# Performance work log

Hardware: AMD Instinct MI355X
Metric: run time of the kernel (lower is better)

The kernel has to match this reference:

```python
import jax, jax.numpy as jnp
import numpy as np

N = 50000
NEG_SLOPE = 0.2

def _gat_layer(x, src, dst, W, a_src, a_dst, b):
    # x: [N, Fin], W: [Fin, Fout], a_src/a_dst: [Fout], b: [Fout]
    h = x @ W                                  # [N, Fout]
    alpha_src = h @ a_src                      # [N]
    alpha_dst = h @ a_dst                      # [N]
    e = alpha_src[src] + alpha_dst[dst]        # [E]
    e = jnp.where(e > 0, e, NEG_SLOPE * e)     # leaky_relu
    # segment softmax over incoming edges of each dst node
    m = jax.ops.segment_max(e, dst, num_segments=N)
    w = jnp.exp(e - m[dst])
    denom = jax.ops.segment_sum(w, dst, num_segments=N) + jnp.asarray(1e-16, e.dtype)
    alpha = w / denom[dst]                     # [E]
    out = jax.ops.segment_sum(alpha[:, None] * h[src], dst, num_segments=N)
    return out + b

def setup_inputs() -> dict:
    key = jax.random.key(0)
    ks = jax.random.split(key, 10)
    x = jax.random.normal(ks[0], (N, 128), dtype=jnp.float32)
    edge_index = jax.random.randint(ks[1], (2, 800000), 0, N, dtype=jnp.int64)
    def glorot(k, shape):
        fan = shape[0] + (shape[1] if len(shape) > 1 else 1)
        s = jnp.sqrt(6.0 / fan)
        return jax.random.uniform(k, shape, jnp.float32, -s, s)
    return {
        "x": x,
        "edge_index": edge_index,
        "W1": glorot(ks[2], (128, 64)),
        "a1_src": glorot(ks[3], (64,)),
        "a1_dst": glorot(ks[4], (64,)),
        "b1": jnp.zeros((64,), jnp.float32),
        "W2": glorot(ks[5], (64, 64)),
        "a2_src": glorot(ks[6], (64,)),
        "a2_dst": glorot(ks[7], (64,)),
        "b2": jnp.zeros((64,), jnp.float32),
    }

def reference(x, edge_index, W1, a1_src, a1_dst, b1, W2, a2_src, a2_dst, b2):
    loops = jnp.arange(N, dtype=edge_index.dtype)
    src = jnp.concatenate([edge_index[0], loops])  # add self-loops (PyG default)
    dst = jnp.concatenate([edge_index[1], loops])
    h = _gat_layer(x, src, dst, W1, a1_src, a1_dst, b1)
    h = jax.nn.relu(h)
    out = _gat_layer(h, src, dst, W2, a2_src, a2_dst, b2)
    return out
```

## Files before the change

### kernel.cpp

```cpp
#include <hip/hip_runtime.h>
#include <hip/hip_bf16.h>
#include <hip/hip_fp16.h>
#include <cstddef>


#define NNODES 50000
#define NEDGES 800000
#define FOUT   64
#define NBKT   512
#define BSPAN  98
#define CHUNK  4096
#define REGS   2560
#define NLBMAX 256

__device__ __forceinline__ float leaky(float t) { return t > 0.f ? t : 0.2f * t; }
#define RL(v, j) __builtin_amdgcn_readlane((v), (j))

using half8  = __attribute__((ext_vector_type(8))) _Float16;
using half4v = __attribute__((ext_vector_type(4))) _Float16;
using f32x4  = __attribute__((ext_vector_type(4))) float;


__global__ __launch_bounds__(256) void k_localsort(
    const int* __restrict__ ei, unsigned* __restrict__ gout,
    int* __restrict__ goff, int E)
{
    __shared__ unsigned lrec[CHUNK];
    __shared__ unsigned lsrt[CHUNK];
    __shared__ int cnt[NBKT];
    __shared__ int cur[NBKT];
    __shared__ int exc[NBKT + 1];

    const int t = threadIdx.x;
    const int blk = blockIdx.x;
    const int e0 = blk * CHUNK;
    const int e1 = min(e0 + CHUNK, E);
    const int ne = e1 - e0;

    for (int i = t; i < NBKT; i += 256) cnt[i] = 0;
    __syncthreads();

    for (int i = e0 + t; i < e1; i += 256) {
        unsigned s = (unsigned)ei[i];
        unsigned d = (unsigned)ei[E + i];
        lrec[i - e0] = s | (d << 16);
        atomicAdd(&cnt[d / BSPAN], 1);
    }
    __syncthreads();

    if (t < 64) {
        int c[8]; int s = 0;
        #pragma unroll
        for (int k = 0; k < 8; ++k) { c[k] = cnt[t * 8 + k]; s += c[k]; }
        int inc = s;
        #pragma unroll
        for (int d = 1; d < 64; d <<= 1) { int u = __shfl_up(inc, d); if (t >= d) inc += u; }
        int ex = inc - s;
        #pragma unroll
        for (int k = 0; k < 8; ++k) { exc[t * 8 + k] = ex; cur[t * 8 + k] = ex; ex += c[k]; }
        if (t == 63) exc[NBKT] = ex;
    }
    __syncthreads();

    for (int i = t; i < ne; i += 256) {
        unsigned r = lrec[i];
        unsigned d = r >> 16;
        unsigned b = d / BSPAN;
        int p = atomicAdd(&cur[b], 1);
        lsrt[p] = (r & 0xFFFFu) | ((d - b * BSPAN) << 16);
    }
    __syncthreads();

    for (int i = t; i < ne; i += 256) gout[e0 + i] = lsrt[i];
    for (int i = t; i < NBKT + 1; i += 256)
        goff[blk * (NBKT + 1) + i] = e0 + exc[i];
}


__device__ __forceinline__ void csr_body(
    char* smem, int bkt,
    const unsigned* __restrict__ gout, const int* __restrict__ goff,
    int* __restrict__ csrc, int2* __restrict__ rowse,
    int n, int nlb)
{
    unsigned* ltmp  = (unsigned*)smem;
    int* lout  = (int*)(smem + REGS * 4);
    int* lcnt  = (int*)(smem + 2 * REGS * 4);
    int* lbase = lcnt + BSPAN;
    int* lcur  = lbase + BSPAN + 1;
    int* rg0   = lcur + BSPAN;
    int* rlen  = rg0 + NLBMAX;
    int* rbase = rlen + NLBMAX;

    const int t = threadIdx.x;
    const int node0 = bkt * BSPAN;
    if (node0 >= n) return;
    const int nn = min(BSPAN, n - node0);

    for (int i = t; i < BSPAN; i += 256) lcnt[i] = (i < nn) ? 1 : 0;
    if (t < nlb) {
        int g0 = goff[t * (NBKT + 1) + bkt];
        int g1 = goff[t * (NBKT + 1) + bkt + 1];
        rg0[t] = g0;
        rlen[t] = g1 - g0;
    }
    __syncthreads();

    if (t < 64) {
        int c[4]; int s = 0;
        #pragma unroll
        for (int k = 0; k < 4; ++k) {
            int idx = t * 4 + k;
            c[k] = (idx < nlb) ? rlen[idx] : 0;
            s += c[k];
        }
        int inc = s;
        #pragma unroll
        for (int d = 1; d < 64; d <<= 1) { int u = __shfl_up(inc, d); if (t >= d) inc += u; }
        int ex = inc - s;
        #pragma unroll
        for (int k = 0; k < 4; ++k) { rbase[t * 4 + k] = ex; ex += c[k]; }
        if (t == 63) rbase[NLBMAX] = ex;
    }
    __syncthreads();

    const int tot = min(rbase[nlb], REGS - BSPAN);

    for (int i = t; i < tot; i += 256) {
        int lo = 0, hi = nlb;
        while (hi - lo > 1) {
            int mid = (lo + hi) >> 1;
            if (rbase[mid] <= i) lo = mid; else hi = mid;
        }
        ltmp[i] = gout[rg0[lo] + (i - rbase[lo])];
    }
    __syncthreads();

    for (int i = t; i < tot; i += 256) atomicAdd(&lcnt[ltmp[i] >> 16], 1);
    __syncthreads();

    if (t < 64) {
        int b0 = t * 2, b1 = t * 2 + 1;
        int c0 = (b0 < BSPAN) ? lcnt[b0] : 0;
        int c1 = (b1 < BSPAN) ? lcnt[b1] : 0;
        int s = c0 + c1;
        int inc = s;
        #pragma unroll
        for (int d = 1; d < 64; d <<= 1) { int u = __shfl_up(inc, d); if (t >= d) inc += u; }
        int ex = inc - s;
        if (b0 < BSPAN) { lbase[b0] = ex;      lcur[b0] = ex + 1; }
        if (b1 < BSPAN) { lbase[b1] = ex + c0; lcur[b1] = ex + c0 + 1; }
        if (t == 63) lbase[BSPAN] = inc;
    }
    __syncthreads();

    for (int i = t; i < nn; i += 256) lout[lbase[i]] = node0 + i;
    for (int i = t; i < tot; i += 256) {
        unsigned r = ltmp[i];
        int p = atomicAdd(&lcur[r >> 16], 1);
        lout[p] = (int)(r & 0xFFFFu);
    }
    __syncthreads();

    const int gbase = bkt * REGS;
    const int total = tot + nn;
    for (int i = t; i < total; i += 256) csrc[gbase + i] = lout[i];
    for (int i = t; i < nn; i += 256)
        rowse[node0 + i] = make_int2(gbase + lbase[i], gbase + lbase[i + 1]);
}


template <int K, typename XT>
__device__ __forceinline__ void gemm_body(
    char* smem, int bx,
    const XT* __restrict__ x, const float* __restrict__ W,
    const float* __restrict__ a_src, const float* __restrict__ a_dst,
    __half* __restrict__ h16, float* __restrict__ as_, float* __restrict__ ad_, int n)
{
    constexpr int KP = K + 8;
    _Float16* Ah = (_Float16*)smem;
    _Float16* Wf = (_Float16*)(smem + 64 * KP * 2);

    const int t    = threadIdx.x;
    const int lane = t & 63;
    const int wv   = t >> 6;
    const int n16  = lane & 15;
    const int quad = lane >> 4;
    const int r0   = bx * 64;

    for (int i = t; i < K * 64; i += 256) {
        int k = i >> 6, c = i & 63;
        Wf[((k >> 3) * 64 + c) * 8 + (k & 7)] = (_Float16)W[i];
    }
    if constexpr (sizeof(XT) == 4) {
        constexpr int KQ = K / 4;
        for (int i = t; i < 64 * KQ; i += 256) {
            int r = i / KQ, kq = i % KQ;
            int row = r0 + r;
            float4 v = make_float4(0.f, 0.f, 0.f, 0.f);
            if (row < n) v = ((const float4*)(x + (size_t)row * K))[kq];
            half4v hv = { (_Float16)v.x, (_Float16)v.y, (_Float16)v.z, (_Float16)v.w };
            *(half4v*)&Ah[r * KP + kq * 4] = hv;
        }
    } else {
        constexpr int KO = K / 8;
        for (int i = t; i < 64 * KO; i += 256) {
            int r = i / KO, ko = i % KO;
            int row = r0 + r;
            half8 hv = {};
            if (row < n) hv = *(const half8*)((const _Float16*)x + (size_t)row * K + ko * 8);
            *(half8*)&Ah[r * KP + ko * 8] = hv;
        }
    }
    __syncthreads();

    half8 bfr[K / 32][4];
    #pragma unroll
    for (int kk = 0; kk < K / 32; ++kk)
        #pragma unroll
        for (int ct = 0; ct < 4; ++ct)
            bfr[kk][ct] = *(const half8*)&Wf[((kk * 4 + quad) * 64 + ct * 16 + n16) * 8];

    f32x4 acc[4];
    #pragma unroll
    for (int ct = 0; ct < 4; ++ct) acc[ct] = (f32x4){0.f, 0.f, 0.f, 0.f};

    #pragma unroll
    for (int kk = 0; kk < K / 32; ++kk) {
        half8 a = *(const half8*)&Ah[(wv * 16 + n16) * KP + kk * 32 + quad * 8];
        #pragma unroll
        for (int ct = 0; ct < 4; ++ct)
            acc[ct] = __builtin_amdgcn_mfma_f32_16x16x32_f16(a, bfr[kk][ct], acc[ct], 0, 0, 0);
    }

    const int rowb = r0 + wv * 16 + quad * 4;
    float asv[4], adv[4];
    #pragma unroll
    for (int ct = 0; ct < 4; ++ct) {
        asv[ct] = a_src[ct * 16 + n16];
        adv[ct] = a_dst[ct * 16 + n16];
    }
    float pa[4] = {0.f, 0.f, 0.f, 0.f}, pd[4] = {0.f, 0.f, 0.f, 0.f};
    #pragma unroll
    for (int ct = 0; ct < 4; ++ct)
        #pragma unroll
        for (int r = 0; r < 4; ++r) {
            pa[r] = fmaf(acc[ct][r], asv[ct], pa[r]);
            pd[r] = fmaf(acc[ct][r], adv[ct], pd[r]);
        }
    #pragma unroll
    for (int r = 0; r < 4; ++r) {
        #pragma unroll
        for (int d = 1; d <= 8; d <<= 1) {
            pa[r] += __shfl_xor(pa[r], d);
            pd[r] += __shfl_xor(pd[r], d);
        }
    }
    if (n16 == 0) {
        #pragma unroll
        for (int r = 0; r < 4; ++r) {
            if (rowb + r < n) { as_[rowb + r] = pa[r]; ad_[rowb + r] = pd[r]; }
        }
    }

    _Float16* hh = (_Float16*)h16;
    #pragma unroll
    for (int r = 0; r < 4; ++r) {
        if (rowb + r < n) {
            #pragma unroll
            for (int ct = 0; ct < 4; ++ct)
                hh[(size_t)(rowb + r) * 64 + ct * 16 + n16] = (_Float16)acc[ct][r];
        }
    }
}


__global__ __launch_bounds__(256) void k_csr_gemm1(
    const unsigned* __restrict__ gout, const int* __restrict__ goff,
    int* __restrict__ csrc, int2* __restrict__ rowse, int nlb,
    const float* __restrict__ x, const float* __restrict__ W1,
    const float* __restrict__ a1s, const float* __restrict__ a1d,
    __half* __restrict__ h16, float* __restrict__ as_, float* __restrict__ ad_, int n)
{
    extern __shared__ __align__(16) char smem[];
    if (blockIdx.x < NBKT)
        csr_body(smem, blockIdx.x, gout, goff, csrc, rowse, n, nlb);
    else
        gemm_body<128, float>(smem, blockIdx.x - NBKT, x, W1, a1s, a1d, h16, as_, ad_, n);
}

__global__ __launch_bounds__(256) void k_gemm2(
    const __half* __restrict__ xh, const float* __restrict__ W2,
    const float* __restrict__ a2s, const float* __restrict__ a2d,
    __half* __restrict__ h16, float* __restrict__ as_, float* __restrict__ ad_, int n)
{
    extern __shared__ __align__(16) char smem[];
    gemm_body<64, _Float16>(smem, blockIdx.x, (const _Float16*)xh, W2, a2s, a2d, h16, as_, ad_, n);
}


template <bool RELU, typename OT>
__device__ __forceinline__ void agg_one(
    int node, int lane, int2* __restrict__ swrow,
    const int2* __restrict__ rowse,
    const int* __restrict__ csrc, const __half* __restrict__ h16,
    const float* __restrict__ as_, const float* __restrict__ ad_,
    const float* __restrict__ bias, OT* __restrict__ out)
{
    const int2 se = rowse[node];
    const int start = se.x;
    const int end   = se.y;
    const int deg   = end - start;
    const float adn = ad_[node];

    if (deg <= 64) {
        int s = 0;
        if (lane < deg) s = csrc[start + lane];
        swrow[lane].x = s << 6;

        const int g  = lane >> 3;
        const int fl = (lane & 7) << 3;
        const __half* __restrict__ hf = h16 + fl;
        const int niter = (deg + 7) >> 3;

        int sofs[8];
        uint4 v[8];
        #pragma unroll
        for (int j = 0; j < 8; ++j) {
            if (j < niter) {
                sofs[j] = swrow[(j << 3) + g].x;
                v[j] = *(const uint4*)(hf + sofs[j]);
            }
        }

        float e = -1e30f;
        if (lane < deg) e = leaky(as_[s] + adn);
        float w = __expf(e);
        float dsum = w;
        #pragma unroll
        for (int d = 32; d >= 1; d >>= 1) dsum += __shfl_xor(dsum, d);
        swrow[lane].y = __float_as_int(w);

        float af[8] = {0.f, 0.f, 0.f, 0.f, 0.f, 0.f, 0.f, 0.f};
        #pragma unroll
        for (int j = 0; j < 8; ++j) {
            if (j < niter) {
                float wj = __int_as_float(swrow[(j << 3) + g].y);
                unsigned uu[4] = {v[j].x, v[j].y, v[j].z, v[j].w};
                #pragma unroll
                for (int q = 0; q < 4; ++q) {
                    __half2 h2 = *(__half2*)&uu[q];
                    float2 f2 = __half22float2(h2);
                    af[2 * q]     = fmaf(wj, f2.x, af[2 * q]);
                    af[2 * q + 1] = fmaf(wj, f2.y, af[2 * q + 1]);
                }
            }
        }
        #pragma unroll
        for (int q = 0; q < 8; ++q) {
            af[q] += __shfl_xor(af[q], 8);
            af[q] += __shfl_xor(af[q], 16);
            af[q] += __shfl_xor(af[q], 32);
        }
        if (g == 0) {
            float inv = 1.f / dsum;
            float4 b0 = *(const float4*)(bias + fl);
            float4 b1 = *(const float4*)(bias + fl + 4);
            float o[8] = { fmaf(af[0], inv, b0.x), fmaf(af[1], inv, b0.y),
                           fmaf(af[2], inv, b0.z), fmaf(af[3], inv, b0.w),
                           fmaf(af[4], inv, b1.x), fmaf(af[5], inv, b1.y),
                           fmaf(af[6], inv, b1.z), fmaf(af[7], inv, b1.w) };
            if (RELU) {
                #pragma unroll
                for (int q = 0; q < 8; ++q) o[q] = fmaxf(o[q], 0.f);
            }
            if constexpr (sizeof(OT) == 2) {
                __half* op = (__half*)out + (size_t)node * 64 + fl;
                __half2 p0 = __floats2half2_rn(o[0], o[1]);
                __half2 p1 = __floats2half2_rn(o[2], o[3]);
                __half2 p2 = __floats2half2_rn(o[4], o[5]);
                __half2 p3 = __floats2half2_rn(o[6], o[7]);
                uint4 pk = { *(unsigned*)&p0, *(unsigned*)&p1, *(unsigned*)&p2, *(unsigned*)&p3 };
                *(uint4*)op = pk;
            } else {
                float* op = (float*)out + (size_t)node * 64 + fl;
                *(float4*)op       = make_float4(o[0], o[1], o[2], o[3]);
                *(float4*)(op + 4) = make_float4(o[4], o[5], o[6], o[7]);
            }
        }
    } else {
        const __half* __restrict__ hp = h16 + lane;
        float m = -1e30f;
        for (int base = start; base < end; base += 64) {
            int idx = base + lane;
            if (idx < end) m = fmaxf(m, leaky(as_[csrc[idx]] + adn));
        }
        #pragma unroll
        for (int d = 32; d >= 1; d >>= 1) m = fmaxf(m, __shfl_xor(m, d));

        float acc0 = 0.f, acc1 = 0.f, acc2 = 0.f, acc3 = 0.f, dsum = 0.f;
        for (int base = start; base < end; base += 64) {
            int idx = base + lane;
            int s = 0; float w = 0.f;
            if (idx < end) {
                s = csrc[idx];
                w = __expf(leaky(as_[s] + adn) - m);
            }
            dsum += w;
            int off = s << 6;
            int wu = __float_as_uint(w);
            int cnt = min(64, end - base);
            int cr = (cnt + 3) & ~3;
            for (int j = 0; j < cr; j += 4) {
                int   o0 = RL(off, j + 0), o1 = RL(off, j + 1);
                int   o2 = RL(off, j + 2), o3 = RL(off, j + 3);
                float w0 = __uint_as_float(RL(wu, j + 0));
                float w1 = __uint_as_float(RL(wu, j + 1));
                float w2 = __uint_as_float(RL(wu, j + 2));
                float w3 = __uint_as_float(RL(wu, j + 3));
                float v0 = __half2float(hp[o0]), v1 = __half2float(hp[o1]);
                float v2 = __half2float(hp[o2]), v3 = __half2float(hp[o3]);
                acc0 = fmaf(w0, v0, acc0);
                acc1 = fmaf(w1, v1, acc1);
                acc2 = fmaf(w2, v2, acc2);
                acc3 = fmaf(w3, v3, acc3);
            }
        }
        #pragma unroll
        for (int d = 32; d >= 1; d >>= 1) dsum += __shfl_xor(dsum, d);
        float acc = (acc0 + acc1) + (acc2 + acc3);
        float o = acc / dsum + bias[lane];
        if (RELU) o = fmaxf(o, 0.f);
        if constexpr (sizeof(OT) == 2)
            ((__half*)out)[(size_t)node * 64 + lane] = __float2half(o);
        else
            ((float*)out)[(size_t)node * 64 + lane] = o;
    }
}

template <bool RELU, typename OT>
__global__ __launch_bounds__(256) void k_aggregate(
    const int2* __restrict__ rowse,
    const int* __restrict__ csrc,
    const __half* __restrict__ h16, const float* __restrict__ as_,
    const float* __restrict__ ad_, const float* __restrict__ bias,
    OT* __restrict__ out, int n)
{
    __shared__ int2 swL[4][64];

    const int lane = threadIdx.x & 63;
    const int wid  = threadIdx.x >> 6;
    const int nodeA = (blockIdx.x * 4 + wid) * 2;
    if (nodeA >= n) return;

    const int half = lane >> 5;
    const int hl   = lane & 31;
    const int node = nodeA + half;

    const int2 se = rowse[node];
    const float adn = ad_[node];
    const int start = se.x;
    const int deg   = se.y - se.x;
    const int mdeg  = max(deg, __shfl_xor(deg, 32));

    if (mdeg <= 32) {
        int s = 0;
        const bool act = hl < deg;
        if (act) s = csrc[start + hl];
        swL[wid][lane].x = s << 6;

        const int g  = (lane >> 3) & 3;
        const int fl = (lane & 7) << 3;
        const __half* __restrict__ hf = h16 + fl;
        int nit = (deg + 3) >> 2;
        nit = max(nit, __shfl_xor(nit, 32));

        const int sbase = (half << 5) + g;
        uint4 v[8];
        #pragma unroll
        for (int j = 0; j < 8; ++j) {
            if (j < nit)
                v[j] = *(const uint4*)(hf + swL[wid][sbase + (j << 2)].x);
        }

        float e = -1e30f;
        if (act) e = leaky(as_[s] + adn);
        float w = __expf(e);
        float dsum = w;
        #pragma unroll
        for (int d = 16; d >= 1; d >>= 1) dsum += __shfl_xor(dsum, d);
        swL[wid][lane].y = __float_as_int(w);

        float af[8] = {0.f, 0.f, 0.f, 0.f, 0.f, 0.f, 0.f, 0.f};
        #pragma unroll
        for (int j = 0; j < 8; ++j) {
            if (j < nit) {
                float wj = __int_as_float(swL[wid][sbase + (j << 2)].y);
                unsigned uu[4] = {v[j].x, v[j].y, v[j].z, v[j].w};
                #pragma unroll
                for (int q = 0; q < 4; ++q) {
                    __half2 h2 = *(__half2*)&uu[q];
                    float2 f2 = __half22float2(h2);
                    af[2 * q]     = fmaf(wj, f2.x, af[2 * q]);
                    af[2 * q + 1] = fmaf(wj, f2.y, af[2 * q + 1]);
                }
            }
        }
        #pragma unroll
        for (int q = 0; q < 8; ++q) {
            af[q] += __shfl_xor(af[q], 8);
            af[q] += __shfl_xor(af[q], 16);
        }
        if (g == 0) {
            float inv = 1.f / dsum;
            float4 b0 = *(const float4*)(bias + fl);
            float4 b1 = *(const float4*)(bias + fl + 4);
            float o[8] = { fmaf(af[0], inv, b0.x), fmaf(af[1], inv, b0.y),
                           fmaf(af[2], inv, b0.z), fmaf(af[3], inv, b0.w),
                           fmaf(af[4], inv, b1.x), fmaf(af[5], inv, b1.y),
                           fmaf(af[6], inv, b1.z), fmaf(af[7], inv, b1.w) };
            if (RELU) {
                #pragma unroll
                for (int q = 0; q < 8; ++q) o[q] = fmaxf(o[q], 0.f);
            }
            if constexpr (sizeof(OT) == 2) {
                __half* op = (__half*)out + (size_t)node * 64 + fl;
                __half2 p0 = __floats2half2_rn(o[0], o[1]);
                __half2 p1 = __floats2half2_rn(o[2], o[3]);
                __half2 p2 = __floats2half2_rn(o[4], o[5]);
                __half2 p3 = __floats2half2_rn(o[6], o[7]);
                uint4 pk = { *(unsigned*)&p0, *(unsigned*)&p1, *(unsigned*)&p2, *(unsigned*)&p3 };
                *(uint4*)op = pk;
            } else {
                float* op = (float*)out + (size_t)node * 64 + fl;
                *(float4*)op       = make_float4(o[0], o[1], o[2], o[3]);
                *(float4*)(op + 4) = make_float4(o[4], o[5], o[6], o[7]);
            }
        }
    } else {
        agg_one<RELU, OT>(nodeA,     lane, swL[wid], rowse, csrc, h16, as_, ad_, bias, out);
        agg_one<RELU, OT>(nodeA + 1, lane, swL[wid], rowse, csrc, h16, as_, ad_, bias, out);
    }
}


extern "C" void kernel_launch(void* const* d_in, const int* in_sizes, int n_in,
                              void* d_out, int out_size, void* d_ws, size_t ws_size,
                              hipStream_t stream) {
    const float* x   = (const float*)d_in[0];
    const int*   ei  = (const int*)  d_in[1];
    const float* W1  = (const float*)d_in[2];
    const float* a1s = (const float*)d_in[3];
    const float* a1d = (const float*)d_in[4];
    const float* b1  = (const float*)d_in[5];
    const float* W2  = (const float*)d_in[6];
    const float* a2s = (const float*)d_in[7];
    const float* a2d = (const float*)d_in[8];
    const float* b2  = (const float*)d_in[9];
    float* out = (float*)d_out;

    const int N_ = NNODES, E_ = NEDGES;
    const int NLB = (E_ + CHUNK - 1) / CHUNK;

    char* ws = (char*)d_ws;
    size_t off = 0;
    auto alloc = [&](size_t bytes) -> void* {
        void* p = ws + off;
        off += (bytes + 255) & ~(size_t)255;
        return p;
    };
    int*      csrc     = (int*)alloc((size_t)NBKT * REGS * 4);
    int2*     rowse    = (int2*)alloc((size_t)N_ * 8);
    float*    as_      = (float*)alloc((size_t)N_ * 4);
    float*    ad_      = (float*)alloc((size_t)N_ * 4);
    __half*   h16      = (__half*)alloc((size_t)N_ * FOUT * 2);
    __half*   xr2h     = (__half*)alloc((size_t)N_ * FOUT * 2);
    unsigned* gout     = (unsigned*)alloc((size_t)E_ * 4);
    int*      goff     = (int*)alloc((size_t)NLB * (NBKT + 1) * 4);

    constexpr unsigned SM_G1 = 64 * (128 + 8) * 2 + 128 * 64 * 2;
    constexpr unsigned SM_G2 = 64 * (64 + 8) * 2  + 64 * 64 * 2;

    const int GB = (N_ + 63) / 64;
    const int AB = (N_ / 2 + 3) / 4;

    k_localsort<<<NLB, 256, 0, stream>>>(ei, gout, goff, E_);
    k_csr_gemm1<<<NBKT + GB, 256, SM_G1, stream>>>(gout, goff, csrc, rowse, NLB,
                                                   x, W1, a1s, a1d, h16, as_, ad_, N_);
    k_aggregate<true,  __half><<<AB, 256, 0, stream>>>(rowse, csrc, h16, as_, ad_, b1, xr2h, N_);
    k_gemm2<<<GB, 256, SM_G2, stream>>>(xr2h, W2, a2s, a2d, h16, as_, ad_, N_);
    k_aggregate<false, float ><<<AB, 256, 0, stream>>>(rowse, csrc, h16, as_, ad_, b2, out, N_);
}
```

Before: 153.8 us.

## Fuse layer-1 aggregation with layer-2 GEMM in one kernel via LDS tile

Merges the first-layer attention aggregation and the second GEMM into a single kernel. Each block aggregates 64 nodes into an fp16 LDS tile, then runs MFMA against W2 and computes the layer-2 attention scalars. This removes one launch and the global write and reread of the intermediate activations. In exchange there are fewer blocks, less parallelism during aggregation, and W2 is reconverted per block. Separate output buffers are used so the kernel does not overwrite h16 while other blocks are still gathering from it.

```diff
diff --git a/kernel.cpp b/kernel.cpp
--- a/kernel.cpp
+++ b/kernel.cpp
@@ -289,13 +289,230 @@
         gemm_body<128, float>(smem, blockIdx.x - NBKT, x, W1, a1s, a1d, h16, as_, ad_, n);
 }
 
-__global__ __launch_bounds__(256) void k_gemm2(
-    const __half* __restrict__ xh, const float* __restrict__ W2,
-    const float* __restrict__ a2s, const float* __restrict__ a2d,
-    __half* __restrict__ h16, float* __restrict__ as_, float* __restrict__ ad_, int n)
+
+__global__ __launch_bounds__(256) void k_agg1_gemm2(
+    const int2* __restrict__ rowse, const int* __restrict__ csrc,
+    const __half* __restrict__ h16, const float* __restrict__ as_,
+    const float* __restrict__ ad_, const float* __restrict__ b1,
+    const float* __restrict__ W2, const float* __restrict__ a2s,
+    const float* __restrict__ a2d,
+    __half* __restrict__ h16b, float* __restrict__ as2_, float* __restrict__ ad2_, int n)
 {
-    extern __shared__ __align__(16) char smem[];
-    gemm_body<64, _Float16>(smem, blockIdx.x, (const _Float16*)xh, W2, a2s, a2d, h16, as_, ad_, n);
+    constexpr int KP = 72;
+    __shared__ __align__(16) _Float16 Ah[64 * KP];
+    __shared__ __align__(16) _Float16 Wf[64 * 64];
+    __shared__ int2 swL[4][64];
+
+    const int t    = threadIdx.x;
+    const int lane = t & 63;
+    const int wid  = t >> 6;
+    const int nt0  = blockIdx.x * 64;
+
+    for (int i = t; i < 64 * 64; i += 256) {
+        int k = i >> 6, c = i & 63;
+        Wf[((k >> 3) * 64 + c) * 8 + (k & 7)] = (_Float16)W2[i];
+    }
+    if (nt0 + 64 > n) {
+        for (int i = t; i < 64 * KP; i += 256) Ah[i] = (_Float16)0.f;
+        __syncthreads();
+    }
+
+    for (int it = 0; it < 8; ++it) {
+        const int nodeA = nt0 + (it * 4 + wid) * 2;
+        if (nodeA >= n) break;
+
+        const int half = lane >> 5;
+        const int hl   = lane & 31;
+        const int node = nodeA + half;
+        const int ln   = node - nt0;
+
+        const int2 se = rowse[node];
+        const float adn = ad_[node];
+        const int start = se.x;
+        const int deg   = se.y - se.x;
+        const int mdeg  = max(deg, __shfl_xor(deg, 32));
+
+        if (mdeg <= 32) {
+            int s = 0;
+            const bool act = hl < deg;
+            if (act) s = csrc[start + hl];
+            swL[wid][lane].x = s << 6;
+
+            const int g  = (lane >> 3) & 3;
+            const int fl = (lane & 7) << 3;
+            const __half* __restrict__ hf = h16 + fl;
+            int nit = (deg + 3) >> 2;
+            nit = max(nit, __shfl_xor(nit, 32));
+
+            const int sbase = (half << 5) + g;
+            uint4 v[8];
+            #pragma unroll
+            for (int j = 0; j < 8; ++j) {
+                if (j < nit)
+                    v[j] = *(const uint4*)(hf + swL[wid][sbase + (j << 2)].x);
+            }
+
+            float e = -1e30f;
+            if (act) e = leaky(as_[s] + adn);
+            float w = __expf(e);
+            float dsum = w;
+            #pragma unroll
+            for (int d = 16; d >= 1; d >>= 1) dsum += __shfl_xor(dsum, d);
+            swL[wid][lane].y = __float_as_int(w);
+
+            float af[8] = {0.f, 0.f, 0.f, 0.f, 0.f, 0.f, 0.f, 0.f};
+            #pragma unroll
+            for (int j = 0; j < 8; ++j) {
+                if (j < nit) {
+                    float wj = __int_as_float(swL[wid][sbase + (j << 2)].y);
+                    unsigned uu[4] = {v[j].x, v[j].y, v[j].z, v[j].w};
+                    #pragma unroll
+                    for (int q = 0; q < 4; ++q) {
+                        __half2 h2 = *(__half2*)&uu[q];
+                        float2 f2 = __half22float2(h2);
+                        af[2 * q]     = fmaf(wj, f2.x, af[2 * q]);
+                        af[2 * q + 1] = fmaf(wj, f2.y, af[2 * q + 1]);
+                    }
+                }
+            }
+            #pragma unroll
+            for (int q = 0; q < 8; ++q) {
+                af[q] += __shfl_xor(af[q], 8);
+                af[q] += __shfl_xor(af[q], 16);
+            }
+            if (g == 0) {
+                float inv = 1.f / dsum;
+                float4 b0 = *(const float4*)(b1 + fl);
+                float4 b4 = *(const float4*)(b1 + fl + 4);
+                float o[8] = { fmaf(af[0], inv, b0.x), fmaf(af[1], inv, b0.y),
+                               fmaf(af[2], inv, b0.z), fmaf(af[3], inv, b0.w),
+                               fmaf(af[4], inv, b4.x), fmaf(af[5], inv, b4.y),
+                               fmaf(af[6], inv, b4.z), fmaf(af[7], inv, b4.w) };
+                #pragma unroll
+                for (int q = 0; q < 8; ++q) o[q] = fmaxf(o[q], 0.f);
+                __half2 p0 = __floats2half2_rn(o[0], o[1]);
+                __half2 p1 = __floats2half2_rn(o[2], o[3]);
+                __half2 p2 = __floats2half2_rn(o[4], o[5]);
+                __half2 p3 = __floats2half2_rn(o[6], o[7]);
+                uint4 pk = { *(unsigned*)&p0, *(unsigned*)&p1, *(unsigned*)&p2, *(unsigned*)&p3 };
+                *(uint4*)&Ah[ln * KP + fl] = pk;
+            }
+        } else {
+            #pragma unroll
+            for (int which = 0; which < 2; ++which) {
+                const int nd = nodeA + which;
+                const int lr = nd - nt0;
+                const int2 se2 = rowse[nd];
+                const int st = se2.x, en = se2.y;
+                const float adn2 = ad_[nd];
+                const __half* __restrict__ hp = h16 + lane;
+
+                float m = -1e30f;
+                for (int base = st; base < en; base += 64) {
+                    int idx = base + lane;
+                    if (idx < en) m = fmaxf(m, leaky(as_[csrc[idx]] + adn2));
+                }
+                #pragma unroll
+                for (int d = 32; d >= 1; d >>= 1) m = fmaxf(m, __shfl_xor(m, d));
+
+                float a0 = 0.f, a1 = 0.f, a2 = 0.f, a3 = 0.f, dsum = 0.f;
+                for (int base = st; base < en; base += 64) {
+                    int idx = base + lane;
+                    int s = 0; float w = 0.f;
+                    if (idx < en) {
+                        s = csrc[idx];
+                        w = __expf(leaky(as_[s] + adn2) - m);
+                    }
+                    dsum += w;
+                    int off = s << 6;
+                    int wu = __float_as_uint(w);
+                    int cnt = min(64, en - base);
+                    int cr = (cnt + 3) & ~3;
+                    for (int j = 0; j < cr; j += 4) {
+                        int   o0 = RL(off, j + 0), o1 = RL(off, j + 1);
+                        int   o2 = RL(off, j + 2), o3 = RL(off, j + 3);
+                        float w0 = __uint_as_float(RL(wu, j + 0));
+                        float w1 = __uint_as_float(RL(wu, j + 1));
+                        float w2 = __uint_as_float(RL(wu, j + 2));
+                        float w3 = __uint_as_float(RL(wu, j + 3));
+                        float v0 = __half2float(hp[o0]), v1 = __half2float(hp[o1]);
+                        float v2 = __half2float(hp[o2]), v3 = __half2float(hp[o3]);
+                        a0 = fmaf(w0, v0, a0);
+                        a1 = fmaf(w1, v1, a1);
+                        a2 = fmaf(w2, v2, a2);
+                        a3 = fmaf(w3, v3, a3);
+                    }
+                }
+                #pragma unroll
+                for (int d = 32; d >= 1; d >>= 1) dsum += __shfl_xor(dsum, d);
+                float o = ((a0 + a1) + (a2 + a3)) / dsum + b1[lane];
+                o = fmaxf(o, 0.f);
+                Ah[lr * KP + lane] = (_Float16)o;
+            }
+        }
+    }
+    __syncthreads();
+
+    const int n16  = lane & 15;
+    const int quad = lane >> 4;
+
+    half8 bfr[2][4];
+    #pragma unroll
+    for (int kk = 0; kk < 2; ++kk)
+        #pragma unroll
+        for (int ct = 0; ct < 4; ++ct)
+            bfr[kk][ct] = *(const half8*)&Wf[((kk * 4 + quad) * 64 + ct * 16 + n16) * 8];
+
+    f32x4 acc[4];
+    #pragma unroll
+    for (int ct = 0; ct < 4; ++ct) acc[ct] = (f32x4){0.f, 0.f, 0.f, 0.f};
+
+    #pragma unroll
+    for (int kk = 0; kk < 2; ++kk) {
+        half8 a = *(const half8*)&Ah[(wid * 16 + n16) * KP + kk * 32 + quad * 8];
+        #pragma unroll
+        for (int ct = 0; ct < 4; ++ct)
+            acc[ct] = __builtin_amdgcn_mfma_f32_16x16x32_f16(a, bfr[kk][ct], acc[ct], 0, 0, 0);
+    }
+
+    const int rowb = nt0 + wid * 16 + quad * 4;
+    float asv[4], adv[4];
+    #pragma unroll
+    for (int ct = 0; ct < 4; ++ct) {
+        asv[ct] = a2s[ct * 16 + n16];
+        adv[ct] = a2d[ct * 16 + n16];
+    }
+    float pa[4] = {0.f, 0.f, 0.f, 0.f}, pd[4] = {0.f, 0.f, 0.f, 0.f};
+    #pragma unroll
+    for (int ct = 0; ct < 4; ++ct)
+        #pragma unroll
+        for (int r = 0; r < 4; ++r) {
+            pa[r] = fmaf(acc[ct][r], asv[ct], pa[r]);
+            pd[r] = fmaf(acc[ct][r], adv[ct], pd[r]);
+        }
+    #pragma unroll
+    for (int r = 0; r < 4; ++r) {
+        #pragma unroll
+        for (int d = 1; d <= 8; d <<= 1) {
+            pa[r] += __shfl_xor(pa[r], d);
+            pd[r] += __shfl_xor(pd[r], d);
+        }
+    }
+    if (n16 == 0) {
+        #pragma unroll
+        for (int r = 0; r < 4; ++r) {
+            if (rowb + r < n) { as2_[rowb + r] = pa[r]; ad2_[rowb + r] = pd[r]; }
+        }
+    }
+    _Float16* hh = (_Float16*)h16b;
+    #pragma unroll
+    for (int r = 0; r < 4; ++r) {
+        if (rowb + r < n) {
+            #pragma unroll
+            for (int ct = 0; ct < 4; ++ct)
+                hh[(size_t)(rowb + r) * 64 + ct * 16 + n16] = (_Float16)acc[ct][r];
+        }
+    }
 }
 
 
@@ -323,14 +540,11 @@
         const __half* __restrict__ hf = h16 + fl;
         const int niter = (deg + 7) >> 3;
 
-        int sofs[8];
         uint4 v[8];
         #pragma unroll
         for (int j = 0; j < 8; ++j) {
-            if (j < niter) {
-                sofs[j] = swrow[(j << 3) + g].x;
-                v[j] = *(const uint4*)(hf + sofs[j]);
-            }
+            if (j < niter)
+                v[j] = *(const uint4*)(hf + swrow[(j << 3) + g].x);
         }
 
         float e = -1e30f;
@@ -365,28 +579,18 @@
         if (g == 0) {
             float inv = 1.f / dsum;
             float4 b0 = *(const float4*)(bias + fl);
-            float4 b1 = *(const float4*)(bias + fl + 4);
+            float4 b1v = *(const float4*)(bias + fl + 4);
             float o[8] = { fmaf(af[0], inv, b0.x), fmaf(af[1], inv, b0.y),
                            fmaf(af[2], inv, b0.z), fmaf(af[3], inv, b0.w),
-                           fmaf(af[4], inv, b1.x), fmaf(af[5], inv, b1.y),
-                           fmaf(af[6], inv, b1.z), fmaf(af[7], inv, b1.w) };
+                           fmaf(af[4], inv, b1v.x), fmaf(af[5], inv, b1v.y),
+                           fmaf(af[6], inv, b1v.z), fmaf(af[7], inv, b1v.w) };
             if (RELU) {
                 #pragma unroll
                 for (int q = 0; q < 8; ++q) o[q] = fmaxf(o[q], 0.f);
             }
-            if constexpr (sizeof(OT) == 2) {
-                __half* op = (__half*)out + (size_t)node * 64 + fl;
-                __half2 p0 = __floats2half2_rn(o[0], o[1]);
-                __half2 p1 = __floats2half2_rn(o[2], o[3]);
-                __half2 p2 = __floats2half2_rn(o[4], o[5]);
-                __half2 p3 = __floats2half2_rn(o[6], o[7]);
-                uint4 pk = { *(unsigned*)&p0, *(unsigned*)&p1, *(unsigned*)&p2, *(unsigned*)&p3 };
-                *(uint4*)op = pk;
-            } else {
-                float* op = (float*)out + (size_t)node * 64 + fl;
-                *(float4*)op       = make_float4(o[0], o[1], o[2], o[3]);
-                *(float4*)(op + 4) = make_float4(o[4], o[5], o[6], o[7]);
-            }
+            float* op = (float*)out + (size_t)node * 64 + fl;
+            *(float4*)op       = make_float4(o[0], o[1], o[2], o[3]);
+            *(float4*)(op + 4) = make_float4(o[4], o[5], o[6], o[7]);
         }
     } else {
         const __half* __restrict__ hp = h16 + lane;
@@ -431,10 +635,7 @@
         float acc = (acc0 + acc1) + (acc2 + acc3);
         float o = acc / dsum + bias[lane];
         if (RELU) o = fmaxf(o, 0.f);
-        if constexpr (sizeof(OT) == 2)
-            ((__half*)out)[(size_t)node * 64 + lane] = __float2half(o);
-        else
-            ((float*)out)[(size_t)node * 64 + lane] = o;
+        ((float*)out)[(size_t)node * 64 + lane] = o;
     }
 }
 
@@ -514,28 +715,18 @@
         if (g == 0) {
             float inv = 1.f / dsum;
             float4 b0 = *(const float4*)(bias + fl);
-            float4 b1 = *(const float4*)(bias + fl + 4);
+            float4 b1v = *(const float4*)(bias + fl + 4);
             float o[8] = { fmaf(af[0], inv, b0.x), fmaf(af[1], inv, b0.y),
                            fmaf(af[2], inv, b0.z), fmaf(af[3], inv, b0.w),
-                           fmaf(af[4], inv, b1.x), fmaf(af[5], inv, b1.y),
-                           fmaf(af[6], inv, b1.z), fmaf(af[7], inv, b1.w) };
+                           fmaf(af[4], inv, b1v.x), fmaf(af[5], inv, b1v.y),
+                           fmaf(af[6], inv, b1v.z), fmaf(af[7], inv, b1v.w) };
             if (RELU) {
                 #pragma unroll
                 for (int q = 0; q < 8; ++q) o[q] = fmaxf(o[q], 0.f);
             }
-            if constexpr (sizeof(OT) == 2) {
-                __half* op = (__half*)out + (size_t)node * 64 + fl;
-                __half2 p0 = __floats2half2_rn(o[0], o[1]);
-                __half2 p1 = __floats2half2_rn(o[2], o[3]);
-                __half2 p2 = __floats2half2_rn(o[4], o[5]);
-                __half2 p3 = __floats2half2_rn(o[6], o[7]);
-                uint4 pk = { *(unsigned*)&p0, *(unsigned*)&p1, *(unsigned*)&p2, *(unsigned*)&p3 };
-                *(uint4*)op = pk;
-            } else {
-                float* op = (float*)out + (size_t)node * 64 + fl;
-                *(float4*)op       = make_float4(o[0], o[1], o[2], o[3]);
-                *(float4*)(op + 4) = make_float4(o[4], o[5], o[6], o[7]);
-            }
+            float* op = (float*)out + (size_t)node * 64 + fl;
+            *(float4*)op       = make_float4(o[0], o[1], o[2], o[3]);
+            *(float4*)(op + 4) = make_float4(o[4], o[5], o[6], o[7]);
         }
     } else {
         agg_one<RELU, OT>(nodeA,     lane, swL[wid], rowse, csrc, h16, as_, ad_, bias, out);
@@ -573,13 +764,14 @@
     int2*     rowse    = (int2*)alloc((size_t)N_ * 8);
     float*    as_      = (float*)alloc((size_t)N_ * 4);
     float*    ad_      = (float*)alloc((size_t)N_ * 4);
+    float*    as2_     = (float*)alloc((size_t)N_ * 4);
+    float*    ad2_     = (float*)alloc((size_t)N_ * 4);
     __half*   h16      = (__half*)alloc((size_t)N_ * FOUT * 2);
-    __half*   xr2h     = (__half*)alloc((size_t)N_ * FOUT * 2);
+    __half*   h16b     = (__half*)alloc((size_t)N_ * FOUT * 2);
     unsigned* gout     = (unsigned*)alloc((size_t)E_ * 4);
     int*      goff     = (int*)alloc((size_t)NLB * (NBKT + 1) * 4);
 
     constexpr unsigned SM_G1 = 64 * (128 + 8) * 2 + 128 * 64 * 2;
-    constexpr unsigned SM_G2 = 64 * (64 + 8) * 2  + 64 * 64 * 2;
 
     const int GB = (N_ + 63) / 64;
     const int AB = (N_ / 2 + 3) / 4;
@@ -587,7 +779,7 @@
     k_localsort<<<NLB, 256, 0, stream>>>(ei, gout, goff, E_);
     k_csr_gemm1<<<NBKT + GB, 256, SM_G1, stream>>>(gout, goff, csrc, rowse, NLB,
                                                    x, W1, a1s, a1d, h16, as_, ad_, N_);
-    k_aggregate<true,  __half><<<AB, 256, 0, stream>>>(rowse, csrc, h16, as_, ad_, b1, xr2h, N_);
-    k_gemm2<<<GB, 256, SM_G2, stream>>>(xr2h, W2, a2s, a2d, h16, as_, ad_, N_);
-    k_aggregate<false, float ><<<AB, 256, 0, stream>>>(rowse, csrc, h16, as_, ad_, b2, out, N_);
+    k_agg1_gemm2<<<GB, 256, 0, stream>>>(rowse, csrc, h16, as_, ad_, b1,
+                                         W2, a2s, a2d, h16b, as2_, ad2_, N_);
+    k_aggregate<false, float><<<AB, 256, 0, stream>>>(rowse, csrc, h16b, as2_, ad2_, b2, out, N_);
 }
```

Measured after the change: 157.3 us. 2.3% more time.
